# Kernel tuning notes

Hardware: AMD Instinct MI355X
Metric: run time of the kernel (lower is better)

Reference implementation:

```python
import jax, jax.numpy as jnp
import numpy as np

# ---- model/problem dimensions (match init_kwargs & input_specs) ----
B, NV, T, C = 2, 975, 48, 128
V, T2 = 3, 12                 # hardcoded in Decoder.loss
L, H, D = 4, 8, 64            # attention_layers, heads, attention_dim
HD = H * D                    # 512
NB, NHID = 6, 4               # RealNVP n_blocks, n_hidden
DIN = (C + 1) * V             # 387, key/value creator input dim
CY = HD + V                   # 515, coupling net input (cond + masked x)
BN = B * (NV // V)            # fused batch*node axis = 650
LOG2PI = float(np.log(2.0 * np.pi))


def _mlp(x, w_in, b_in, w_hid, b_hid, w_out, b_out, act):
    # [Linear] + n_hidden*[act, Linear] + [act, Linear_out]  (RealNVP s/t nets)
    h = x @ w_in + b_in
    for i in range(w_hid.shape[0]):
        h = act(h) @ w_hid[i] + b_hid[i]
    return act(h) @ w_out + b_out


def _ln(x, s, b, eps=1e-5):
    m = jnp.mean(x, -1, keepdims=True)
    v = jnp.mean((x - m) ** 2, -1, keepdims=True)
    return (x - m) * jax.lax.rsqrt(v + eps) * s + b


def setup_inputs() -> dict:
    key = jax.random.key(0)
    ks = iter(jax.random.split(key, 40))
    rn = lambda shape, s=0.05: s * jax.random.normal(next(ks), shape, jnp.float32)
    return dict(
        encoded=rn((B, NV, T, C), 1.0),
        true_value=rn((B, NV, T), 1.0),
        W_shift=rn((V * C, HD)), b_shift=rn((HD,)),
        W_key=rn((L, H, DIN, D)), b_key=rn((L, H, D)),
        W_val=rn((L, H, DIN, D)), b_val=rn((L, H, D)),
        ln1_s=jnp.ones((L, HD)), ln1_b=jnp.zeros((L, HD)),
        ff_w1=rn((L, HD, HD)), ff_b1=rn((L, HD)),
        ff_w2=rn((L, HD, HD)), ff_b2=rn((L, HD)),
        ln2_s=jnp.ones((L, HD)), ln2_b=jnp.zeros((L, HD)),
        s_w_in=rn((NB, CY, HD)), s_b_in=rn((NB, HD)),
        s_w_hid=rn((NB, NHID, HD, HD)), s_b_hid=rn((NB, NHID, HD)),
        s_w_out=rn((NB, HD, V)), s_b_out=rn((NB, V)),
        t_w_in=rn((NB, CY, HD)), t_b_in=rn((NB, HD)),
        t_w_hid=rn((NB, NHID, HD, HD)), t_b_hid=rn((NB, NHID, HD)),
        t_w_out=rn((NB, HD, V)), t_b_out=rn((NB, V)),
        bn_log_gamma=jnp.zeros((NB, V)), bn_beta=jnp.zeros((NB, V)),
    )


def reference(encoded, true_value, W_shift, b_shift, W_key, b_key, W_val, b_val,
              ln1_s, ln1_b, ff_w1, ff_b1, ff_w2, ff_b2, ln2_s, ln2_b,
              s_w_in, s_b_in, s_w_hid, s_b_hid, s_w_out, s_b_out,
              t_w_in, t_b_in, t_w_hid, t_b_hid, t_w_out, t_b_out,
              bn_log_gamma, bn_beta):
    b, nv, t, c = encoded.shape
    bn_ = b * (nv // V)
    enc = encoded.reshape(bn_, V, t, c)
    tv = true_value.reshape(bn_, V, t)

    # encoded_value: concat true value, interleave variables per timestep
    ev = jnp.concatenate([enc, tv[..., None]], -1)              # [bn,V,t,c+1]
    ev = ev.transpose(0, 2, 1, 3).reshape(bn_, t, V * (c + 1))  # [bn,t,387]

    # all layers/heads K,V in one batched GEMM each: [L,bn,H,t,D]
    keys = jnp.einsum('bte,lhed->lbhtd', ev, W_key) + b_key[:, None, :, None, :]
    vals = jnp.einsum('bte,lhed->lbhtd', ev, W_val) + b_val[:, None, :, None, :]

    # queries from last t2 encoded steps
    att_in = enc[:, :, -T2:, :].transpose(0, 2, 1, 3).reshape(bn_, T2, V * c)
    att_value = att_in @ W_shift + b_shift                      # [bn,T2,HD]

    # tril(inf).flip((2,3)) mask: key index w is masked iff w >= (t - T2) + v
    qi = jnp.arange(T2)[:, None]
    ki = jnp.arange(t)[None, :]
    masked = ki >= (t - T2) + qi                                # [T2,t]
    scale = D ** (-0.5)

    for l in range(L):
        q = att_value.reshape(bn_, T2, H, D)
        scores = jnp.einsum('bvhi,bhwi->bhvw', q, keys[l])
        scores = jnp.where(masked, -jnp.inf, scores) * scale
        w = jax.nn.softmax(scores, axis=-1)
        att = jnp.einsum('bhvw,bhwj->bvhj', w, vals[l]).reshape(bn_, T2, HD)
        att_value = _ln(att_value + att, ln1_s[l], ln1_b[l])    # dropout = eval/no-op
        ff = jax.nn.relu(att_value @ ff_w1[l] + ff_b1[l]) @ ff_w2[l] + ff_b2[l]
        att_value = _ln(att_value + ff, ln2_s[l], ln2_b[l])

    # RealNVP log_prob of last T2 true values, conditioned on att_value
    x = tv[:, :, -T2:].transpose(0, 2, 1)                       # [bn,T2,V]
    y = att_value                                               # [bn,T2,HD]
    u = x
    log_det = jnp.zeros_like(x)
    eps = 1e-5
    for blk in range(NB):
        mask = ((jnp.arange(V) + blk) % 2).astype(u.dtype)      # alternating
        mu = u * mask
        inp = jnp.concatenate([y, mu], -1)                      # [bn,T2,515]
        s = _mlp(inp, s_w_in[blk], s_b_in[blk], s_w_hid[blk], s_b_hid[blk],
                 s_w_out[blk], s_b_out[blk], jnp.tanh)
        tr = _mlp(inp, t_w_in[blk], t_b_in[blk], t_w_hid[blk], t_b_hid[blk],
                  t_w_out[blk], t_b_out[blk], jax.nn.relu)
        u = mu + (1.0 - mask) * (u - tr) * jnp.exp(-s)
        log_det = log_det - (1.0 - mask) * s
        # batch-norm flow (training-mode batch statistics over dim 0)
        bm = jnp.mean(u, axis=0)                                # [T2,V]
        bv = jnp.mean((u - bm) ** 2, axis=0)
        u = jnp.exp(bn_log_gamma[blk]) * (u - bm) * jax.lax.rsqrt(bv + eps) + bn_beta[blk]
        log_det = log_det + (bn_log_gamma[blk] - 0.5 * jnp.log(bv + eps))

    lp = -0.5 * u * u - 0.5 * LOG2PI + log_det                  # [bn,T2,V]
    log_prob = lp.sum(-1)                                       # [bn,T2]
    return -log_prob.sum(1)                                     # [bn]
```

## Files before the change

### kernel.cpp

```cpp
#include <hip/hip_runtime.h>
#include <math.h>

#define BN_ 650
#define T_ 48
#define V_ 3
#define T2_ 12
#define NROWS_ 7800
#define MKV_ 31200
#define LOG2PI_ 1.8378770664093453f

typedef short s8v __attribute__((ext_vector_type(8)));
typedef float f4v __attribute__((ext_vector_type(4)));

__device__ __forceinline__ float b2f(unsigned short h) {
  return __uint_as_float(((unsigned)h) << 16);
}
__device__ __forceinline__ unsigned short f2b(float f) {
  unsigned u = __float_as_uint(f);
  return (unsigned short)((u + 0x7fffu + ((u >> 16) & 1u)) >> 16);
}

struct GZ {
  const unsigned short* A;
  const unsigned short* B;
  const float* bias;
  unsigned short* C;
  const unsigned short* res;
  int act;
};

template<int BM>
__global__ __launch_bounds__(256)
void gemm_bf16(GZ g0, GZ g1, int M, int Kp)
{
  constexpr int MF = BM / 32;
  constexpr int AU = BM / 32;
  __shared__ __align__(16) unsigned short As[2][BM * 72];
  __shared__ __align__(16) unsigned short Bs[2][128 * 72];
  GZ g = (blockIdx.z == 0) ? g0 : g1;
  const int tid = threadIdx.x;
  const int lane = tid & 63;
  const int wid = tid >> 6;
  const int wm = wid >> 1, wn = wid & 1;
  const int m0 = blockIdx.y * BM, n0 = blockIdx.x * 128;
  const int fr = lane & 15, fko = (lane >> 4) * 8;

  f4v acc[MF][4];
  #pragma unroll
  for (int i = 0; i < MF; i++)
    #pragma unroll
    for (int j = 0; j < 4; j++) acc[i][j] = (f4v){0.f, 0.f, 0.f, 0.f};

  const int steps = Kp >> 6;
  s8v ra[AU], rb[4];
  const s8v zed = (s8v){0,0,0,0,0,0,0,0};

  int arow[AU], akseg[AU], brow[4], bkseg[4];
  #pragma unroll
  for (int i = 0; i < AU; i++) { int gx = tid*AU + i; arow[i] = gx >> 3; akseg[i] = (gx & 7) * 8; }
  #pragma unroll
  for (int i = 0; i < 4; i++) { int gx = tid*4 + i; brow[i] = gx >> 3; bkseg[i] = (gx & 7) * 8; }

  #pragma unroll
  for (int i = 0; i < AU; i++)
    ra[i] = (m0 + arow[i] < M) ? *(const s8v*)(g.A + (size_t)(m0 + arow[i])*Kp + akseg[i]) : zed;
  #pragma unroll
  for (int i = 0; i < 4; i++)
    rb[i] = *(const s8v*)(g.B + (size_t)(n0 + brow[i])*Kp + bkseg[i]);
  #pragma unroll
  for (int i = 0; i < AU; i++) *(s8v*)&As[0][arow[i]*72 + akseg[i]] = ra[i];
  #pragma unroll
  for (int i = 0; i < 4; i++)  *(s8v*)&Bs[0][brow[i]*72 + bkseg[i]] = rb[i];
  __syncthreads();

  for (int s = 0; s < steps; s++) {
    if (s + 1 < steps) {
      const int ko = (s + 1) * 64;
      #pragma unroll
      for (int i = 0; i < AU; i++)
        ra[i] = (m0 + arow[i] < M) ? *(const s8v*)(g.A + (size_t)(m0 + arow[i])*Kp + ko + akseg[i]) : zed;
      #pragma unroll
      for (int i = 0; i < 4; i++)
        rb[i] = *(const s8v*)(g.B + (size_t)(n0 + brow[i])*Kp + ko + bkseg[i]);
    }
    const int buf = s & 1;
    #pragma unroll
    for (int kk = 0; kk < 2; kk++) {
      s8v af[MF], bfr[4];
      #pragma unroll
      for (int mm = 0; mm < MF; mm++)
        af[mm] = *(const s8v*)&As[buf][(wm*(BM/2) + mm*16 + fr)*72 + kk*32 + fko];
      #pragma unroll
      for (int nn = 0; nn < 4; nn++)
        bfr[nn] = *(const s8v*)&Bs[buf][(wn*64 + nn*16 + fr)*72 + kk*32 + fko];
      #pragma unroll
      for (int mm = 0; mm < MF; mm++)
        #pragma unroll
        for (int nn = 0; nn < 4; nn++)
          acc[mm][nn] = __builtin_amdgcn_mfma_f32_16x16x32_bf16(af[mm], bfr[nn], acc[mm][nn], 0, 0, 0);
    }
    if (s + 1 < steps) {
      #pragma unroll
      for (int i = 0; i < AU; i++) *(s8v*)&As[buf^1][arow[i]*72 + akseg[i]] = ra[i];
      #pragma unroll
      for (int i = 0; i < 4; i++)  *(s8v*)&Bs[buf^1][brow[i]*72 + bkseg[i]] = rb[i];
    }
    __syncthreads();
  }

  unsigned short* cs = &As[0][0];
  #pragma unroll
  for (int mm = 0; mm < MF; mm++) {
    #pragma unroll
    for (int nn = 0; nn < 4; nn++) {
      const int col = wn*64 + nn*16 + fr;
      const int gcol = n0 + col;
      const int row0 = wm*(BM/2) + mm*16 + (lane >> 4)*4;
      const float bc = g.bias ? g.bias[gcol] : 0.f;
      #pragma unroll
      for (int q = 0; q < 4; q++) {
        const int r = m0 + row0 + q;
        float v = acc[mm][nn][q] + bc;
        if (g.act == 1) v = fmaxf(v, 0.f);
        else if (g.act == 2) v = tanhf(v);
        if (g.res && r < M) v += b2f(g.res[(size_t)r*512 + gcol]);
        cs[(row0 + q)*136 + col] = f2b(v);
      }
    }
  }
  __syncthreads();
  for (int ch = tid; ch < BM*16; ch += 256) {
    const int row = ch >> 4, c8 = ch & 15;
    const int r = m0 + row;
    if (r < M)
      *(s8v*)(g.C + (size_t)r*512 + n0 + c8*8) = *(const s8v*)&cs[row*136 + c8*8];
  }
}

__global__ __launch_bounds__(512)
void gemm_kv(const unsigned short* __restrict__ A, const unsigned short* __restrict__ B,
             const float* __restrict__ kb, const float* __restrict__ vb,
             unsigned short* __restrict__ C, int M)
{
  __shared__ __align__(16) unsigned short Al[128*456];
  __shared__ __align__(16) unsigned short Bst[2][128*72];
  const int tid = threadIdx.x;
  const int lane = tid & 63, wid = tid >> 6;
  const int wm = wid >> 1, wn = wid & 1;
  const int m0 = blockIdx.x * 128;
  const int fr = lane & 15, fko = (lane >> 4) * 8;
  const s8v zed = (s8v){0,0,0,0,0,0,0,0};

  #pragma unroll
  for (int i = 0; i < 14; i++) {
    const int idx = tid + i*512;
    const int row = idx / 56, c8 = idx - row*56;
    const s8v v = (m0 + row < M) ? *(const s8v*)(A + (size_t)(m0 + row)*448 + c8*8) : zed;
    *(s8v*)&Al[row*456 + c8*8] = v;
  }

  int brow[2], bkseg[2];
  #pragma unroll
  for (int i = 0; i < 2; i++) { const int gx = tid*2 + i; brow[i] = gx >> 3; bkseg[i] = (gx & 7)*8; }

  for (int ns = 0; ns < 8; ns++) {
    const unsigned short* Bn = B + (size_t)ns*128*448;
    s8v rb[2];
    #pragma unroll
    for (int i = 0; i < 2; i++)
      rb[i] = *(const s8v*)(Bn + (size_t)brow[i]*448 + bkseg[i]);
    #pragma unroll
    for (int i = 0; i < 2; i++) *(s8v*)&Bst[0][brow[i]*72 + bkseg[i]] = rb[i];
    __syncthreads();

    f4v acc[2][4];
    #pragma unroll
    for (int i = 0; i < 2; i++)
      #pragma unroll
      for (int j = 0; j < 4; j++) acc[i][j] = (f4v){0.f, 0.f, 0.f, 0.f};

    for (int s = 0; s < 7; s++) {
      if (s + 1 < 7) {
        const int ko = (s + 1)*64;
        #pragma unroll
        for (int i = 0; i < 2; i++)
          rb[i] = *(const s8v*)(Bn + (size_t)brow[i]*448 + ko + bkseg[i]);
      }
      const int buf = s & 1;
      #pragma unroll
      for (int kk = 0; kk < 2; kk++) {
        s8v af[2], bfr[4];
        #pragma unroll
        for (int mm = 0; mm < 2; mm++)
          af[mm] = *(const s8v*)&Al[(wm*32 + mm*16 + fr)*456 + s*64 + kk*32 + fko];
        #pragma unroll
        for (int nn = 0; nn < 4; nn++)
          bfr[nn] = *(const s8v*)&Bst[buf][(wn*64 + nn*16 + fr)*72 + kk*32 + fko];
        #pragma unroll
        for (int mm = 0; mm < 2; mm++)
          #pragma unroll
          for (int nn = 0; nn < 4; nn++)
            acc[mm][nn] = __builtin_amdgcn_mfma_f32_16x16x32_bf16(af[mm], bfr[nn], acc[mm][nn], 0, 0, 0);
      }
      if (s + 1 < 7) {
        #pragma unroll
        for (int i = 0; i < 2; i++) *(s8v*)&Bst[buf^1][brow[i]*72 + bkseg[i]] = rb[i];
      }
      __syncthreads();
    }

    unsigned short* cs = &Bst[0][0];
    #pragma unroll
    for (int mm = 0; mm < 2; mm++) {
      #pragma unroll
      for (int nn = 0; nn < 4; nn++) {
        const int col = wn*64 + nn*16 + fr;
        const int cg = ns*128 + col;
        const int row0 = wm*32 + mm*16 + (lane >> 4)*4;
        const float bc = (cg < 512) ? kb[cg] : vb[cg - 512];
        #pragma unroll
        for (int q = 0; q < 4; q++)
          cs[(row0 + q)*136 + col] = f2b(acc[mm][nn][q] + bc);
      }
    }
    __syncthreads();
    #pragma unroll
    for (int i = 0; i < 4; i++) {
      const int ch = tid + i*512;
      const int row = ch >> 4, c8 = ch & 15;
      const int r = m0 + row;
      if (r < M)
        *(s8v*)(C + (size_t)r*1024 + ns*128 + c8*8) = *(const s8v*)&cs[row*136 + c8*8];
    }
    __syncthreads();
  }
}

__global__ void prep_evb(const float* __restrict__ enc, const float* __restrict__ tv,
                         unsigned short* __restrict__ evb)
{
  const int r = blockIdx.x;
  const int bn = r / 48, t = r - bn * 48;
  for (int col = threadIdx.x; col < 448; col += 256) {
    unsigned short o = 0;
    if (col < 387) {
      const int v = col / 129, cc = col - v * 129;
      const float val = (cc < 128) ? enc[(((size_t)bn*3 + v)*48 + t)*128 + cc]
                                   : tv[((size_t)bn*3 + v)*48 + t];
      o = f2b(val);
    }
    evb[(size_t)r*448 + col] = o;
  }
}

__global__ void prep_attb(const float* __restrict__ enc, unsigned short* __restrict__ attb)
{
  const int r = blockIdx.x;
  const int bn = r / 12, q = r - bn * 12;
  for (int col = threadIdx.x; col < 384; col += 256) {
    const int v = col >> 7, cc = col & 127;
    attb[(size_t)r*384 + col] = f2b(enc[(((size_t)bn*3 + v)*48 + 36 + q)*128 + cc]);
  }
}

__global__ void prep_wkv(const float* __restrict__ Wk, const float* __restrict__ Wv,
                         unsigned short* __restrict__ WT)
{
  const int l = blockIdx.y, n = blockIdx.x;
  const int kvs = n >> 9, h = (n >> 6) & 7, d = n & 63;
  const float* src = (kvs ? Wv : Wk) + ((size_t)(l*8 + h)*387)*64 + d;
  unsigned short* dst = WT + ((size_t)l*1024 + n)*448;
  for (int k = threadIdx.x; k < 448; k += 256)
    dst[k] = (k < 387) ? f2b(src[(size_t)k*64]) : 0;
}

__global__ void prep_wsh(const float* __restrict__ W, unsigned short* __restrict__ WT)
{
  const int n = blockIdx.x;
  for (int k = threadIdx.x; k < 384; k += 256)
    WT[(size_t)n*384 + k] = f2b(W[(size_t)k*512 + n]);
}

__global__ void prep_wff(const float* __restrict__ W1, const float* __restrict__ W2,
                         unsigned short* __restrict__ T1, unsigned short* __restrict__ T2b)
{
  const int n = blockIdx.x, l = blockIdx.y, which = blockIdx.z;
  const float* src = (which ? W2 : W1) + (size_t)l*512*512;
  unsigned short* dst = (which ? T2b : T1) + ((size_t)l*512 + n)*512;
  for (int k = threadIdx.x; k < 512; k += 256)
    dst[k] = f2b(src[(size_t)k*512 + n]);
}

__global__ void prep_wnvp_in(const float* __restrict__ Ws, const float* __restrict__ Wt,
                             unsigned short* __restrict__ Ts, unsigned short* __restrict__ Tt)
{
  const int n = blockIdx.x, blk = blockIdx.y, net = blockIdx.z;
  const float* src = (net ? Wt : Ws) + (size_t)blk*515*512;
  unsigned short* dst = (net ? Tt : Ts) + ((size_t)blk*512 + n)*576;
  for (int k = threadIdx.x; k < 576; k += 256)
    dst[k] = (k < 515) ? f2b(src[(size_t)k*512 + n]) : 0;
}

__global__ void prep_wnvp_hid(const float* __restrict__ Ws, const float* __restrict__ Wt,
                              unsigned short* __restrict__ Ts, unsigned short* __restrict__ Tt)
{
  const int n = blockIdx.x, bi = blockIdx.y, net = blockIdx.z;
  const float* src = (net ? Wt : Ws) + (size_t)bi*512*512;
  unsigned short* dst = (net ? Tt : Ts) + ((size_t)bi*512 + n)*512;
  for (int k = threadIdx.x; k < 512; k += 256)
    dst[k] = f2b(src[(size_t)k*512 + n]);
}

__global__ void pad_ab_kernel(unsigned short* __restrict__ ab)
{
  const int r = blockIdx.x;
  if (threadIdx.x < 64) ab[(size_t)r*576 + 512 + threadIdx.x] = 0;
}

__global__ void zero_stats_kernel(float* __restrict__ sraw)
{
  const int i = blockIdx.x * blockDim.x + threadIdx.x;
  if (i < 6*36*2) sraw[i] = 0.f;
}

__global__ __launch_bounds__(512)
void attn_kernel(const unsigned short* __restrict__ avb, const unsigned short* __restrict__ kvb,
                 const float* __restrict__ lns, const float* __restrict__ lnb,
                 unsigned short* __restrict__ av2b)
{
  const int b = blockIdx.x, tid = threadIdx.x;
  const int h = tid >> 6, lane = tid & 63;
  __shared__ float av [12][516];
  __shared__ float att[12][516];
  __shared__ unsigned short vsh[8][48][68];

  for (int idx = tid; idx < 12*64; idx += 512) {
    const int v = idx >> 6, c8 = idx & 63;
    const s8v a8 = *(const s8v*)(avb + (((size_t)b*12 + v) << 9) + c8*8);
    #pragma unroll
    for (int j = 0; j < 8; j++) av[v][c8*8 + j] = b2f((unsigned short)a8[j]);
  }
  {
    const int t0 = lane >> 3, c8 = lane & 7;
    #pragma unroll
    for (int i = 0; i < 6; i++) {
      const int t = i*8 + t0;
      *(s8v*)&vsh[h][t][c8*8] =
          *(const s8v*)(kvb + (size_t)(b*48 + t)*1024 + 512 + h*64 + c8*8);
    }
  }
  __syncthreads();

  const int tcl = (lane < 48) ? lane : 0;
  s8v kp[8];
  {
    const unsigned short* kr = kvb + (size_t)(b*48 + tcl)*1024 + h*64;
    #pragma unroll
    for (int i = 0; i < 8; i++) kp[i] = *(const s8v*)(kr + i*8);
  }

  float p[12];
  #pragma unroll
  for (int v = 0; v < 12; v++) p[v] = 0.f;
  #pragma unroll
  for (int k8 = 0; k8 < 8; k8++) {
    float kf[8];
    #pragma unroll
    for (int j = 0; j < 8; j++) kf[j] = b2f((unsigned short)kp[k8][j]);
    #pragma unroll
    for (int v = 0; v < 12; v++) {
      const float* qp = &av[v][h*64 + k8*8];
      #pragma unroll
      for (int j = 0; j < 8; j++) p[v] = fmaf(qp[j], kf[j], p[v]);
    }
  }
  #pragma unroll
  for (int v = 0; v < 12; v++) {
    const bool valid = (lane < 36 + v);
    float s = valid ? p[v]*0.125f : -1e30f;
    float m = s;
    #pragma unroll
    for (int off = 1; off < 64; off <<= 1) m = fmaxf(m, __shfl_xor(m, off));
    const float e = valid ? expf(s - m) : 0.f;
    float sum = e;
    #pragma unroll
    for (int off = 1; off < 64; off <<= 1) sum += __shfl_xor(sum, off);
    p[v] = e / sum;
  }
  float o[12];
  #pragma unroll
  for (int v = 0; v < 12; v++) o[v] = 0.f;
  #pragma unroll
  for (int t6 = 0; t6 < 6; t6++) {
    float vf[8];
    #pragma unroll
    for (int j = 0; j < 8; j++) vf[j] = b2f(vsh[h][t6*8 + j][lane]);
    #pragma unroll
    for (int j = 0; j < 8; j++) {
      const int tt = t6*8 + j;
      #pragma unroll
      for (int v = 0; v < 12; v++) o[v] = fmaf(__shfl(p[v], tt), vf[j], o[v]);
    }
  }
  #pragma unroll
  for (int v = 0; v < 12; v++) att[v][h*64 + lane] = o[v];
  __syncthreads();

  for (int v = h; v < 12; v += 8) {
    float x[8], sm = 0.f, s2 = 0.f;
    #pragma unroll
    for (int j = 0; j < 8; j++) {
      const int c = lane*8 + j;
      const float t = av[v][c] + att[v][c];
      x[j] = t; sm += t; s2 += t*t;
    }
    #pragma unroll
    for (int off = 32; off; off >>= 1) { sm += __shfl_xor(sm, off); s2 += __shfl_xor(s2, off); }
    const float mean = sm * (1.f/512.f);
    const float var  = s2 * (1.f/512.f) - mean*mean;
    const float rr = rsqrtf(var + 1e-5f);
    #pragma unroll
    for (int j = 0; j < 8; j++) {
      const int c = lane*8 + j;
      av2b[(((size_t)b*12 + v) << 9) + c] = f2b((x[j] - mean)*rr*lns[c] + lnb[c]);
    }
  }
}

__global__ __launch_bounds__(256)
void ln_kernel(const unsigned short* __restrict__ in, unsigned short* __restrict__ out, int ldo,
               const float* __restrict__ s, const float* __restrict__ b)
{
  const int row = blockIdx.x*4 + (threadIdx.x >> 6);
  const int lane = threadIdx.x & 63;
  const s8v xv = *(const s8v*)(in + (size_t)row*512 + lane*8);
  float x[8], sm = 0.f, s2 = 0.f;
  #pragma unroll
  for (int j = 0; j < 8; j++) {
    const float t = b2f((unsigned short)xv[j]);
    x[j] = t; sm += t; s2 += t*t;
  }
  #pragma unroll
  for (int o = 32; o; o >>= 1) { sm += __shfl_xor(sm, o); s2 += __shfl_xor(s2, o); }
  const float mean = sm * (1.f/512.f);
  const float var  = s2 * (1.f/512.f) - mean*mean;
  const float rr = rsqrtf(var + 1e-5f);
  s8v o8;
  #pragma unroll
  for (int j = 0; j < 8; j++) {
    const int c = lane*8 + j;
    o8[j] = (short)f2b((x[j] - mean)*rr*s[c] + b[c]);
  }
  *(s8v*)(out + (size_t)row*ldo + lane*8) = o8;
}

__global__ void mu_kernel(const float* __restrict__ tv, const float* __restrict__ u,
                          const float* __restrict__ sab, float* __restrict__ uinf,
                          unsigned short* __restrict__ ab, int blk)
{
  const int r = blockIdx.x*256 + threadIdx.x;
  if (r >= NROWS_) return;
  const int bn = r / 12, q = r - bn * 12;
  float uv[3];
  #pragma unroll
  for (int v = 0; v < 3; v++) {
    if (blk == 0) uv[v] = tv[((size_t)bn*3 + v)*48 + 36 + q];
    else {
      const float a = sab[((blk-1)*36 + q*3 + v)*2 + 0];
      const float c = sab[((blk-1)*36 + q*3 + v)*2 + 1];
      uv[v] = fmaf(a, u[(size_t)r*3 + v], c);
    }
  }
  #pragma unroll
  for (int v = 0; v < 3; v++) {
    uinf[(size_t)r*3 + v] = uv[v];
    ab[(size_t)r*576 + 512 + v] = f2b(((v + blk) & 1) ? uv[v] : 0.f);
  }
}

__global__ __launch_bounds__(512)
void out_couple_kernel(const unsigned short* __restrict__ hs, const unsigned short* __restrict__ ht,
                const float* __restrict__ swo, const float* __restrict__ sbo,
                const float* __restrict__ two, const float* __restrict__ tbo,
                const float* __restrict__ uinf, float* __restrict__ u, float* __restrict__ ld,
                float* __restrict__ sraw, int blk)
{
  __shared__ float sres[4][2][3];
  const int tid = threadIdx.x;
  const int w = tid >> 6, lane = tid & 63;
  const int rloc = w >> 1, net = w & 1;
  const int r = blockIdx.x*4 + rloc;
  const unsigned short* hrow = (net ? ht : hs) + ((size_t)r << 9);
  const float* wo = (net ? two : swo) + (size_t)blk*512*3;

  const s8v hv8 = *(const s8v*)(hrow + lane*8);
  float wbuf[24];
  #pragma unroll
  for (int i = 0; i < 6; i++)
    *(float4*)&wbuf[i*4] = *(const float4*)(wo + lane*24 + i*4);
  float a0 = 0.f, a1 = 0.f, a2 = 0.f;
  #pragma unroll
  for (int i = 0; i < 8; i++) {
    const float hv = b2f((unsigned short)hv8[i]);
    a0 = fmaf(hv, wbuf[i*3+0], a0);
    a1 = fmaf(hv, wbuf[i*3+1], a1);
    a2 = fmaf(hv, wbuf[i*3+2], a2);
  }
  #pragma unroll
  for (int o = 32; o; o >>= 1) {
    a0 += __shfl_xor(a0, o); a1 += __shfl_xor(a1, o); a2 += __shfl_xor(a2, o);
  }
  if (lane == 0) {
    const float* bo = (net ? tbo : sbo) + blk*3;
    sres[rloc][net][0] = a0 + bo[0];
    sres[rloc][net][1] = a1 + bo[1];
    sres[rloc][net][2] = a2 + bo[2];
  }
  __syncthreads();
  if (tid < 12) {
    const int rl = tid / 3, j = tid - 3*rl;
    const int r2 = blockIdx.x*4 + rl;
    const int q = r2 % 12;
    const int msk = (j + blk) & 1;
    const float s = sres[rl][0][j];
    const float t = sres[rl][1][j];
    const float uo = uinf[(size_t)r2*3 + j];
    const float unew = msk ? uo : (uo - t) * expf(-s);
    u[(size_t)r2*3 + j] = unew;
    const float prev = blk ? ld[(size_t)r2*3 + j] : 0.f;
    ld[(size_t)r2*3 + j] = prev - (msk ? 0.f : s);
    atomicAdd(&sraw[(blk*36 + q*3 + j)*2 + 0], unew);
    atomicAdd(&sraw[(blk*36 + q*3 + j)*2 + 1], unew * unew);
  }
}

__global__ void bn_finalize_kernel(const float* __restrict__ sraw, float* __restrict__ sab,
    float* __restrict__ ldadd, const float* __restrict__ lg, const float* __restrict__ bt, int blk)
{
  const int idx = threadIdx.x;
  if (idx < 36) {
    const int v = idx % 3;
    const float sum = sraw[(blk*36 + idx)*2 + 0];
    const float s2  = sraw[(blk*36 + idx)*2 + 1];
    const float bm  = sum * (1.f / 650.f);
    const float bvr = s2 * (1.f / 650.f) - bm * bm;
    const float g = lg[blk*3 + v];
    const float a = expf(g) * rsqrtf(bvr + 1e-5f);
    sab[(blk*36 + idx)*2 + 0] = a;
    sab[(blk*36 + idx)*2 + 1] = bt[blk*3 + v] - a * bm;
    ldadd[blk*36 + idx] = g - 0.5f * logf(bvr + 1e-5f);
  }
}

__global__ void loss_kernel(const float* __restrict__ u, const float* __restrict__ ld,
    const float* __restrict__ sab, const float* __restrict__ ldadd, float* __restrict__ out)
{
  const int bn = blockIdx.x * blockDim.x + threadIdx.x;
  if (bn >= BN_) return;
  float acc = 0.f;
  for (int t2 = 0; t2 < 12; t2++) {
    #pragma unroll
    for (int v = 0; v < 3; v++) {
      const int idx = t2*3 + v;
      const float a = sab[(5*36 + idx)*2 + 0];
      const float c = sab[(5*36 + idx)*2 + 1];
      const float ur = u[((size_t)bn*12 + t2)*3 + v];
      const float ub = fmaf(a, ur, c);
      acc += 0.5f*ub*ub + 0.5f*LOG2PI_ - ld[((size_t)bn*12 + t2)*3 + v];
    }
  }
  float lsum = 0.f;
  for (int i = 0; i < 6*36; i++) lsum += ldadd[i];
  out[bn] = acc - lsum;
}

#define O_WKV    (size_t)0
#define O_WSH    (size_t)3670016
#define O_WFF1   (size_t)4063232
#define O_WFF2   (size_t)6160384
#define O_WSIN   (size_t)8257536
#define O_WTIN   (size_t)11796480
#define O_WSHID  (size_t)15335424
#define O_WTHID  (size_t)27918336
#define O_EVB    (size_t)40501248
#define O_ATTB   (size_t)68456448
#define O_AVB    (size_t)74446848
#define O_AV2B   (size_t)82434048
#define O_HB     (size_t)90421248
#define O_FFSUM  (size_t)98408448
#define O_KVB    (size_t)106395648
#define O_AB     O_KVB
#define O_HS0    (O_KVB + 8985600)
#define O_HS1    (O_HS0 + 7987200)
#define O_HT0    (O_HS1 + 7987200)
#define O_HT1    (O_HT0 + 7987200)
#define O_UINF   (size_t)170293248
#define O_U      (size_t)170386848
#define O_LD     (size_t)170480448
#define O_SRAW   (size_t)170761248
#define O_SAB    (size_t)170762976
#define O_LDA    (size_t)170764704

static inline GZ mkgz(const void* A, const void* B, const float* bias, void* C,
                      const void* res, int act) {
  GZ g; g.A = (const unsigned short*)A; g.B = (const unsigned short*)B; g.bias = bias;
  g.C = (unsigned short*)C; g.res = (const unsigned short*)res; g.act = act; return g;
}

extern "C" void kernel_launch(void* const* d_in, const int* in_sizes, int n_in,
                              void* d_out, int out_size, void* d_ws, size_t ws_size,
                              hipStream_t stream)
{
  const float* enc   = (const float*)d_in[0];
  const float* tv    = (const float*)d_in[1];
  const float* Wsh   = (const float*)d_in[2];
  const float* bsh   = (const float*)d_in[3];
  const float* Wk    = (const float*)d_in[4];
  const float* bk    = (const float*)d_in[5];
  const float* Wv    = (const float*)d_in[6];
  const float* bv    = (const float*)d_in[7];
  const float* ln1s  = (const float*)d_in[8];
  const float* ln1b  = (const float*)d_in[9];
  const float* fw1   = (const float*)d_in[10];
  const float* fb1   = (const float*)d_in[11];
  const float* fw2   = (const float*)d_in[12];
  const float* fb2   = (const float*)d_in[13];
  const float* ln2s  = (const float*)d_in[14];
  const float* ln2b  = (const float*)d_in[15];
  const float* swin  = (const float*)d_in[16];
  const float* sbin  = (const float*)d_in[17];
  const float* swhid = (const float*)d_in[18];
  const float* sbhid = (const float*)d_in[19];
  const float* swout = (const float*)d_in[20];
  const float* sbout = (const float*)d_in[21];
  const float* twin  = (const float*)d_in[22];
  const float* tbin  = (const float*)d_in[23];
  const float* twhid = (const float*)d_in[24];
  const float* tbhid = (const float*)d_in[25];
  const float* twout = (const float*)d_in[26];
  const float* tbout = (const float*)d_in[27];
  const float* bnlg  = (const float*)d_in[28];
  const float* bnbt  = (const float*)d_in[29];

  char* ws = (char*)d_ws;
  unsigned short* wkv   = (unsigned short*)(ws + O_WKV);
  unsigned short* wsht  = (unsigned short*)(ws + O_WSH);
  unsigned short* wff1t = (unsigned short*)(ws + O_WFF1);
  unsigned short* wff2t = (unsigned short*)(ws + O_WFF2);
  unsigned short* wsint = (unsigned short*)(ws + O_WSIN);
  unsigned short* wtint = (unsigned short*)(ws + O_WTIN);
  unsigned short* wshid = (unsigned short*)(ws + O_WSHID);
  unsigned short* wthid = (unsigned short*)(ws + O_WTHID);
  unsigned short* evb   = (unsigned short*)(ws + O_EVB);
  unsigned short* attb  = (unsigned short*)(ws + O_ATTB);
  unsigned short* avb   = (unsigned short*)(ws + O_AVB);
  unsigned short* av2b  = (unsigned short*)(ws + O_AV2B);
  unsigned short* hb    = (unsigned short*)(ws + O_HB);
  unsigned short* ffsum = (unsigned short*)(ws + O_FFSUM);
  unsigned short* kvb   = (unsigned short*)(ws + O_KVB);
  unsigned short* ab    = (unsigned short*)(ws + O_AB);
  unsigned short* hs0   = (unsigned short*)(ws + O_HS0);
  unsigned short* hs1   = (unsigned short*)(ws + O_HS1);
  unsigned short* ht0   = (unsigned short*)(ws + O_HT0);
  unsigned short* ht1   = (unsigned short*)(ws + O_HT1);
  float* uinf  = (float*)(ws + O_UINF);
  float* u     = (float*)(ws + O_U);
  float* ld    = (float*)(ws + O_LD);
  float* sraw  = (float*)(ws + O_SRAW);
  float* sab   = (float*)(ws + O_SAB);
  float* lda   = (float*)(ws + O_LDA);
  float* out   = (float*)d_out;

  prep_evb<<<MKV_, 256, 0, stream>>>(enc, tv, evb);
  prep_attb<<<NROWS_, 256, 0, stream>>>(enc, attb);
  prep_wkv<<<dim3(1024, 4), 256, 0, stream>>>(Wk, Wv, wkv);
  prep_wsh<<<512, 256, 0, stream>>>(Wsh, wsht);
  prep_wff<<<dim3(512, 4, 2), 256, 0, stream>>>(fw1, fw2, wff1t, wff2t);
  prep_wnvp_in<<<dim3(512, 6, 2), 256, 0, stream>>>(swin, twin, wsint, wtint);
  prep_wnvp_hid<<<dim3(512, 24, 2), 256, 0, stream>>>(swhid, twhid, wshid, wthid);
  zero_stats_kernel<<<2, 256, 0, stream>>>(sraw);

  const GZ gnull = mkgz(nullptr, nullptr, nullptr, nullptr, nullptr, 0);

  {
    GZ g = mkgz(attb, wsht, bsh, avb, nullptr, 0);
    gemm_bf16<128><<<dim3(4, 61, 1), 256, 0, stream>>>(g, gnull, NROWS_, 384);
  }

  for (int l = 0; l < 4; l++) {
    gemm_kv<<<244, 512, 0, stream>>>(evb, wkv + (size_t)l*1024*448,
        bk + l*512, bv + l*512, kvb, MKV_);
    attn_kernel<<<BN_, 512, 0, stream>>>(avb, kvb, ln1s + l*512, ln1b + l*512, av2b);
    GZ g1 = mkgz(av2b, wff1t + (size_t)l*512*512, fb1 + l*512, hb, nullptr, 1);
    gemm_bf16<128><<<dim3(4, 61, 1), 256, 0, stream>>>(g1, gnull, NROWS_, 512);
    GZ g2 = mkgz(hb, wff2t + (size_t)l*512*512, fb2 + l*512, ffsum, av2b, 0);
    gemm_bf16<128><<<dim3(4, 61, 1), 256, 0, stream>>>(g2, gnull, NROWS_, 512);
    if (l == 3)
      ln_kernel<<<1950, 256, 0, stream>>>(ffsum, ab, 576, ln2s + l*512, ln2b + l*512);
    else
      ln_kernel<<<1950, 256, 0, stream>>>(ffsum, avb, 512, ln2s + l*512, ln2b + l*512);
  }

  pad_ab_kernel<<<NROWS_, 64, 0, stream>>>(ab);
  for (int blk = 0; blk < 6; blk++) {
    mu_kernel<<<31, 256, 0, stream>>>(tv, u, sab, uinf, ab, blk);
    {
      GZ gs = mkgz(ab, wsint + (size_t)blk*512*576, sbin + blk*512, hs0, nullptr, 2);
      GZ gt = mkgz(ab, wtint + (size_t)blk*512*576, tbin + blk*512, ht0, nullptr, 1);
      gemm_bf16<128><<<dim3(4, 61, 2), 256, 0, stream>>>(gs, gt, NROWS_, 576);
    }
    for (int i = 0; i < 4; i++) {
      unsigned short* srcs = (i & 1) ? hs1 : hs0;
      unsigned short* dsts = (i & 1) ? hs0 : hs1;
      unsigned short* srct = (i & 1) ? ht1 : ht0;
      unsigned short* dstt = (i & 1) ? ht0 : ht1;
      GZ gs = mkgz(srcs, wshid + (size_t)(blk*4 + i)*512*512, sbhid + (blk*4 + i)*512, dsts, nullptr, 2);
      GZ gt = mkgz(srct, wthid + (size_t)(blk*4 + i)*512*512, tbhid + (blk*4 + i)*512, dstt, nullptr, 1);
      gemm_bf16<128><<<dim3(4, 61, 2), 256, 0, stream>>>(gs, gt, NROWS_, 512);
    }
    out_couple_kernel<<<1950, 512, 0, stream>>>(hs0, ht0, swout, sbout, twout, tbout,
        uinf, u, ld, sraw, blk);
    bn_finalize_kernel<<<1, 64, 0, stream>>>(sraw, sab, lda, bnlg, bnbt, blk);
  }
  loss_kernel<<<3, 256, 0, stream>>>(u, ld, sab, lda, out);
}
```

Before: 2.161 ms.

## Add 256x256-tile GEMM for RealNVP coupling nets and shrink attention LDS to bf16

```diff
diff --git a/kernel.cpp b/kernel.cpp
--- a/kernel.cpp
+++ b/kernel.cpp
@@ -134,6 +134,109 @@
     const int r = m0 + row;
     if (r < M)
       *(s8v*)(g.C + (size_t)r*512 + n0 + c8*8) = *(const s8v*)&cs[row*136 + c8*8];
+  }
+}
+
+__global__ __launch_bounds__(512)
+void gemm256(GZ g0, GZ g1, int M, int Kp)
+{
+  __shared__ __align__(16) unsigned short As[2][256 * 72];
+  __shared__ __align__(16) unsigned short Bs[2][256 * 72];
+  GZ g = (blockIdx.z == 0) ? g0 : g1;
+  const int tid = threadIdx.x;
+  const int lane = tid & 63;
+  const int wid = tid >> 6;
+  const int wm = wid >> 2, wn = wid & 3;
+  const int m0 = blockIdx.y * 256, n0 = blockIdx.x * 256;
+  const int fr = lane & 15, fko = (lane >> 4) * 8;
+
+  f4v acc[8][4];
+  #pragma unroll
+  for (int i = 0; i < 8; i++)
+    #pragma unroll
+    for (int j = 0; j < 4; j++) acc[i][j] = (f4v){0.f, 0.f, 0.f, 0.f};
+
+  const int steps = Kp >> 6;
+  s8v ra[4], rb[4];
+  const s8v zed = (s8v){0,0,0,0,0,0,0,0};
+
+  int arow[4], akseg[4];
+  #pragma unroll
+  for (int i = 0; i < 4; i++) { int gx = tid*4 + i; arow[i] = gx >> 3; akseg[i] = (gx & 7) * 8; }
+
+  #pragma unroll
+  for (int i = 0; i < 4; i++)
+    ra[i] = (m0 + arow[i] < M) ? *(const s8v*)(g.A + (size_t)(m0 + arow[i])*Kp + akseg[i]) : zed;
+  #pragma unroll
+  for (int i = 0; i < 4; i++)
+    rb[i] = *(const s8v*)(g.B + (size_t)(n0 + arow[i])*Kp + akseg[i]);
+  #pragma unroll
+  for (int i = 0; i < 4; i++) *(s8v*)&As[0][arow[i]*72 + akseg[i]] = ra[i];
+  #pragma unroll
+  for (int i = 0; i < 4; i++) *(s8v*)&Bs[0][arow[i]*72 + akseg[i]] = rb[i];
+  __syncthreads();
+
+  for (int s = 0; s < steps; s++) {
+    if (s + 1 < steps) {
+      const int ko = (s + 1) * 64;
+      #pragma unroll
+      for (int i = 0; i < 4; i++)
+        ra[i] = (m0 + arow[i] < M) ? *(const s8v*)(g.A + (size_t)(m0 + arow[i])*Kp + ko + akseg[i]) : zed;
+      #pragma unroll
+      for (int i = 0; i < 4; i++)
+        rb[i] = *(const s8v*)(g.B + (size_t)(n0 + arow[i])*Kp + ko + akseg[i]);
+    }
+    const int buf = s & 1;
+    #pragma unroll
+    for (int kk = 0; kk < 2; kk++) {
+      s8v af[8], bfr[4];
+      #pragma unroll
+      for (int mm = 0; mm < 8; mm++)
+        af[mm] = *(const s8v*)&As[buf][(wm*128 + mm*16 + fr)*72 + kk*32 + fko];
+      #pragma unroll
+      for (int nn = 0; nn < 4; nn++)
+        bfr[nn] = *(const s8v*)&Bs[buf][(wn*64 + nn*16 + fr)*72 + kk*32 + fko];
+      #pragma unroll
+      for (int mm = 0; mm < 8; mm++)
+        #pragma unroll
+        for (int nn = 0; nn < 4; nn++)
+          acc[mm][nn] = __builtin_amdgcn_mfma_f32_16x16x32_bf16(af[mm], bfr[nn], acc[mm][nn], 0, 0, 0);
+    }
+    if (s + 1 < steps) {
+      #pragma unroll
+      for (int i = 0; i < 4; i++) *(s8v*)&As[buf^1][arow[i]*72 + akseg[i]] = ra[i];
+      #pragma unroll
+      for (int i = 0; i < 4; i++) *(s8v*)&Bs[buf^1][arow[i]*72 + akseg[i]] = rb[i];
+    }
+    __syncthreads();
+  }
+
+  unsigned short* cs = &As[0][0];
+  #pragma unroll
+  for (int mm = 0; mm < 8; mm++) {
+    #pragma unroll
+    for (int nn = 0; nn < 4; nn++) {
+      const int col = wn*64 + nn*16 + fr;
+      const int gcol = n0 + col;
+      const int row0 = wm*128 + mm*16 + (lane >> 4)*4;
+      const float bc = g.bias ? g.bias[gcol] : 0.f;
+      #pragma unroll
+      for (int q = 0; q < 4; q++) {
+        const int r = m0 + row0 + q;
+        float v = acc[mm][nn][q] + bc;
+        if (g.act == 1) v = fmaxf(v, 0.f);
+        else if (g.act == 2) v = tanhf(v);
+        if (g.res && r < M) v += b2f(g.res[(size_t)r*512 + gcol]);
+        cs[(row0 + q)*264 + col] = f2b(v);
+      }
+    }
+  }
+  __syncthreads();
+  for (int ch = tid; ch < 256*32; ch += 512) {
+    const int row = ch >> 5, c8 = ch & 31;
+    const int r = m0 + row;
+    if (r < M)
+      *(s8v*)(g.C + (size_t)r*512 + n0 + c8*8) = *(const s8v*)&cs[row*264 + c8*8];
   }
 }
 
@@ -330,15 +433,13 @@
 {
   const int b = blockIdx.x, tid = threadIdx.x;
   const int h = tid >> 6, lane = tid & 63;
-  __shared__ float av [12][516];
-  __shared__ float att[12][516];
+  __shared__ unsigned short avs [12][520];
+  __shared__ unsigned short atts[12][520];
   __shared__ unsigned short vsh[8][48][68];
 
   for (int idx = tid; idx < 12*64; idx += 512) {
     const int v = idx >> 6, c8 = idx & 63;
-    const s8v a8 = *(const s8v*)(avb + (((size_t)b*12 + v) << 9) + c8*8);
-    #pragma unroll
-    for (int j = 0; j < 8; j++) av[v][c8*8 + j] = b2f((unsigned short)a8[j]);
+    *(s8v*)&avs[v][c8*8] = *(const s8v*)(avb + (((size_t)b*12 + v) << 9) + c8*8);
   }
   {
     const int t0 = lane >> 3, c8 = lane & 7;
@@ -369,9 +470,9 @@
     for (int j = 0; j < 8; j++) kf[j] = b2f((unsigned short)kp[k8][j]);
     #pragma unroll
     for (int v = 0; v < 12; v++) {
-      const float* qp = &av[v][h*64 + k8*8];
-      #pragma unroll
-      for (int j = 0; j < 8; j++) p[v] = fmaf(qp[j], kf[j], p[v]);
+      const s8v q8 = *(const s8v*)&avs[v][h*64 + k8*8];
+      #pragma unroll
+      for (int j = 0; j < 8; j++) p[v] = fmaf(b2f((unsigned short)q8[j]), kf[j], p[v]);
     }
   }
   #pragma unroll
@@ -403,15 +504,16 @@
     }
   }
   #pragma unroll
-  for (int v = 0; v < 12; v++) att[v][h*64 + lane] = o[v];
+  for (int v = 0; v < 12; v++) atts[v][h*64 + lane] = f2b(o[v]);
   __syncthreads();
 
   for (int v = h; v < 12; v += 8) {
     float x[8], sm = 0.f, s2 = 0.f;
+    const s8v a8 = *(const s8v*)&avs[v][lane*8];
+    const s8v t8 = *(const s8v*)&atts[v][lane*8];
     #pragma unroll
     for (int j = 0; j < 8; j++) {
-      const int c = lane*8 + j;
-      const float t = av[v][c] + att[v][c];
+      const float t = b2f((unsigned short)a8[j]) + b2f((unsigned short)t8[j]);
       x[j] = t; sm += t; s2 += t*t;
     }
     #pragma unroll
@@ -707,7 +809,7 @@
     {
       GZ gs = mkgz(ab, wsint + (size_t)blk*512*576, sbin + blk*512, hs0, nullptr, 2);
       GZ gt = mkgz(ab, wtint + (size_t)blk*512*576, tbin + blk*512, ht0, nullptr, 1);
-      gemm_bf16<128><<<dim3(4, 61, 2), 256, 0, stream>>>(gs, gt, NROWS_, 576);
+      gemm256<<<dim3(2, 31, 2), 512, 0, stream>>>(gs, gt, NROWS_, 576);
     }
     for (int i = 0; i < 4; i++) {
       unsigned short* srcs = (i & 1) ? hs1 : hs0;
@@ -716,7 +818,7 @@
       unsigned short* dstt = (i & 1) ? ht0 : ht1;
       GZ gs = mkgz(srcs, wshid + (size_t)(blk*4 + i)*512*512, sbhid + (blk*4 + i)*512, dsts, nullptr, 2);
       GZ gt = mkgz(srct, wthid + (size_t)(blk*4 + i)*512*512, tbhid + (blk*4 + i)*512, dstt, nullptr, 1);
-      gemm_bf16<128><<<dim3(4, 61, 2), 256, 0, stream>>>(gs, gt, NROWS_, 512);
+      gemm256<<<dim3(2, 31, 2), 512, 0, stream>>>(gs, gt, NROWS_, 512);
     }
     out_couple_kernel<<<1950, 512, 0, stream>>>(hs0, ht0, swout, sbout, twout, tbout,
         uinf, u, ld, sraw, blk);
```

Measured after the change: 2.809 ms. 30.0% more time.

## Use tiled shared-memory transpose for weight prep and bf16 attention smem

Applied to the files above, without the earlier changes.

```diff
diff --git a/kernel.cpp b/kernel.cpp
--- a/kernel.cpp
+++ b/kernel.cpp
@@ -236,6 +236,37 @@
   }
 }
 
+__global__ __launch_bounds__(256)
+void trans_w(const float* __restrict__ src, unsigned short* __restrict__ dst,
+             int K, int N, int Kp, int ktiles, size_t sstride, size_t dstride)
+{
+  __shared__ float tile[64][65];
+  const int kt = blockIdx.x % ktiles, nt = blockIdx.x / ktiles;
+  const int k0 = kt*64, n0 = nt*64;
+  const float* s = src + (size_t)blockIdx.y * sstride;
+  unsigned short* d = dst + (size_t)blockIdx.y * dstride;
+  const int tid = threadIdx.x;
+  const int r = tid >> 4, c4 = (tid & 15) * 4;
+  #pragma unroll
+  for (int i = 0; i < 4; i++) {
+    const int k = k0 + r + i*16;
+    float4 v = {0.f, 0.f, 0.f, 0.f};
+    if (k < K) v = *(const float4*)(s + (size_t)k*N + n0 + c4);
+    tile[r + i*16][c4+0] = v.x; tile[r + i*16][c4+1] = v.y;
+    tile[r + i*16][c4+2] = v.z; tile[r + i*16][c4+3] = v.w;
+  }
+  __syncthreads();
+  const int n = tid >> 2, kk0 = (tid & 3) * 16;
+  #pragma unroll
+  for (int i = 0; i < 2; i++) {
+    s8v o;
+    #pragma unroll
+    for (int j = 0; j < 8; j++)
+      o[j] = (short)f2b(tile[kk0 + i*8 + j][n]);
+    *(s8v*)(d + (size_t)(n0 + n)*Kp + k0 + kk0 + i*8) = o;
+  }
+}
+
 __global__ void prep_evb(const float* __restrict__ enc, const float* __restrict__ tv,
                          unsigned short* __restrict__ evb)
 {
@@ -274,43 +305,6 @@
     dst[k] = (k < 387) ? f2b(src[(size_t)k*64]) : 0;
 }
 
-__global__ void prep_wsh(const float* __restrict__ W, unsigned short* __restrict__ WT)
-{
-  const int n = blockIdx.x;
-  for (int k = threadIdx.x; k < 384; k += 256)
-    WT[(size_t)n*384 + k] = f2b(W[(size_t)k*512 + n]);
-}
-
-__global__ void prep_wff(const float* __restrict__ W1, const float* __restrict__ W2,
-                         unsigned short* __restrict__ T1, unsigned short* __restrict__ T2b)
-{
-  const int n = blockIdx.x, l = blockIdx.y, which = blockIdx.z;
-  const float* src = (which ? W2 : W1) + (size_t)l*512*512;
-  unsigned short* dst = (which ? T2b : T1) + ((size_t)l*512 + n)*512;
-  for (int k = threadIdx.x; k < 512; k += 256)
-    dst[k] = f2b(src[(size_t)k*512 + n]);
-}
-
-__global__ void prep_wnvp_in(const float* __restrict__ Ws, const float* __restrict__ Wt,
-                             unsigned short* __restrict__ Ts, unsigned short* __restrict__ Tt)
-{
-  const int n = blockIdx.x, blk = blockIdx.y, net = blockIdx.z;
-  const float* src = (net ? Wt : Ws) + (size_t)blk*515*512;
-  unsigned short* dst = (net ? Tt : Ts) + ((size_t)blk*512 + n)*576;
-  for (int k = threadIdx.x; k < 576; k += 256)
-    dst[k] = (k < 515) ? f2b(src[(size_t)k*512 + n]) : 0;
-}
-
-__global__ void prep_wnvp_hid(const float* __restrict__ Ws, const float* __restrict__ Wt,
-                              unsigned short* __restrict__ Ts, unsigned short* __restrict__ Tt)
-{
-  const int n = blockIdx.x, bi = blockIdx.y, net = blockIdx.z;
-  const float* src = (net ? Wt : Ws) + (size_t)bi*512*512;
-  unsigned short* dst = (net ? Tt : Ts) + ((size_t)bi*512 + n)*512;
-  for (int k = threadIdx.x; k < 512; k += 256)
-    dst[k] = f2b(src[(size_t)k*512 + n]);
-}
-
 __global__ void pad_ab_kernel(unsigned short* __restrict__ ab)
 {
   const int r = blockIdx.x;
@@ -330,15 +324,13 @@
 {
   const int b = blockIdx.x, tid = threadIdx.x;
   const int h = tid >> 6, lane = tid & 63;
-  __shared__ float av [12][516];
-  __shared__ float att[12][516];
+  __shared__ unsigned short avs [12][520];
+  __shared__ unsigned short atts[12][520];
   __shared__ unsigned short vsh[8][48][68];
 
   for (int idx = tid; idx < 12*64; idx += 512) {
     const int v = idx >> 6, c8 = idx & 63;
-    const s8v a8 = *(const s8v*)(avb + (((size_t)b*12 + v) << 9) + c8*8);
-    #pragma unroll
-    for (int j = 0; j < 8; j++) av[v][c8*8 + j] = b2f((unsigned short)a8[j]);
+    *(s8v*)&avs[v][c8*8] = *(const s8v*)(avb + (((size_t)b*12 + v) << 9) + c8*8);
   }
   {
     const int t0 = lane >> 3, c8 = lane & 7;
@@ -369,9 +361,9 @@
     for (int j = 0; j < 8; j++) kf[j] = b2f((unsigned short)kp[k8][j]);
     #pragma unroll
     for (int v = 0; v < 12; v++) {
-      const float* qp = &av[v][h*64 + k8*8];
-      #pragma unroll
-      for (int j = 0; j < 8; j++) p[v] = fmaf(qp[j], kf[j], p[v]);
+      const s8v q8 = *(const s8v*)&avs[v][h*64 + k8*8];
+      #pragma unroll
+      for (int j = 0; j < 8; j++) p[v] = fmaf(b2f((unsigned short)q8[j]), kf[j], p[v]);
     }
   }
   #pragma unroll
@@ -403,15 +395,16 @@
     }
   }
   #pragma unroll
-  for (int v = 0; v < 12; v++) att[v][h*64 + lane] = o[v];
+  for (int v = 0; v < 12; v++) atts[v][h*64 + lane] = f2b(o[v]);
   __syncthreads();
 
   for (int v = h; v < 12; v += 8) {
     float x[8], sm = 0.f, s2 = 0.f;
+    const s8v a8 = *(const s8v*)&avs[v][lane*8];
+    const s8v t8 = *(const s8v*)&atts[v][lane*8];
     #pragma unroll
     for (int j = 0; j < 8; j++) {
-      const int c = lane*8 + j;
-      const float t = av[v][c] + att[v][c];
+      const float t = b2f((unsigned short)a8[j]) + b2f((unsigned short)t8[j]);
       x[j] = t; sm += t; s2 += t*t;
     }
     #pragma unroll
@@ -674,10 +667,20 @@
   prep_evb<<<MKV_, 256, 0, stream>>>(enc, tv, evb);
   prep_attb<<<NROWS_, 256, 0, stream>>>(enc, attb);
   prep_wkv<<<dim3(1024, 4), 256, 0, stream>>>(Wk, Wv, wkv);
-  prep_wsh<<<512, 256, 0, stream>>>(Wsh, wsht);
-  prep_wff<<<dim3(512, 4, 2), 256, 0, stream>>>(fw1, fw2, wff1t, wff2t);
-  prep_wnvp_in<<<dim3(512, 6, 2), 256, 0, stream>>>(swin, twin, wsint, wtint);
-  prep_wnvp_hid<<<dim3(512, 24, 2), 256, 0, stream>>>(swhid, twhid, wshid, wthid);
+  trans_w<<<dim3(6*8, 1),  256, 0, stream>>>(Wsh,  wsht,  384, 512, 384, 6,
+      (size_t)0, (size_t)0);
+  trans_w<<<dim3(8*8, 4),  256, 0, stream>>>(fw1,  wff1t, 512, 512, 512, 8,
+      (size_t)512*512, (size_t)512*512);
+  trans_w<<<dim3(8*8, 4),  256, 0, stream>>>(fw2,  wff2t, 512, 512, 512, 8,
+      (size_t)512*512, (size_t)512*512);
+  trans_w<<<dim3(9*8, 6),  256, 0, stream>>>(swin, wsint, 515, 512, 576, 9,
+      (size_t)515*512, (size_t)512*576);
+  trans_w<<<dim3(9*8, 6),  256, 0, stream>>>(twin, wtint, 515, 512, 576, 9,
+      (size_t)515*512, (size_t)512*576);
+  trans_w<<<dim3(8*8, 24), 256, 0, stream>>>(swhid, wshid, 512, 512, 512, 8,
+      (size_t)512*512, (size_t)512*512);
+  trans_w<<<dim3(8*8, 24), 256, 0, stream>>>(twhid, wthid, 512, 512, 512, 8,
+      (size_t)512*512, (size_t)512*512);
   zero_stats_kernel<<<2, 256, 0, stream>>>(sraw);
 
   const GZ gnull = mkgz(nullptr, nullptr, nullptr, nullptr, nullptr, 0);
```

Result: faster. 2.075 ms (-4.0%).
